# Kernel optimization log

Measured on AMD Instinct MI355X. Metric: run time of the kernel, lower is better.

The kernel has to match this reference:

```python
import jax, jax.numpy as jnp
import numpy as np

B, S, DIM, H = 2, 2048, 1536, 12
HD = DIM // H  # 128
EPS = 1e-6


def setup_inputs() -> dict:
    key = jax.random.key(0)
    ks = jax.random.split(key, 6)
    x = jax.random.normal(ks[0], (B, S, DIM), dtype=jnp.float32)
    # RoPE rotation as (cos, sin) pairs: shape [S, 1, HD//2, 2]
    inv = 1.0 / (10000.0 ** (np.arange(0, HD, 2, dtype=np.float32) / HD))
    ang = np.arange(S, dtype=np.float32)[:, None] * inv[None, :]  # [S, HD//2]
    freqs = jnp.asarray(np.stack([np.cos(ang), np.sin(ang)], axis=-1))[:, None, :, :]
    def lin(k):
        return jax.random.normal(k, (DIM, DIM), dtype=jnp.float32) * 0.02
    wq, wk, wv, wo = lin(ks[1]), lin(ks[2]), lin(ks[3]), lin(ks[4])
    zb = jnp.zeros((DIM,), dtype=jnp.float32)
    ones = jnp.ones((DIM,), dtype=jnp.float32)
    return dict(x=x, freqs=freqs,
                wq=wq, bq=zb, wk=wk, bk=zb, wv=wv, bv=zb, wo=wo, bo=zb,
                gq=ones, gk=ones, timestep=500)


def reference(x, freqs, wq, bq, wk, bk, wv, bv, wo, bo, gq, gk, timestep):
    b, s, dim = x.shape

    def rms(z, g):
        zf = z.astype(jnp.float32)
        n = zf * jax.lax.rsqrt(jnp.mean(zf * zf, axis=-1, keepdims=True) + EPS)
        return n.astype(z.dtype) * g

    def rope(t):
        # [b,s,dim] -> [b,s,H,HD//2,2] pairs; complex multiply by freqs
        tp = t.reshape(b, s, H, HD // 2, 2)
        tr, ti = tp[..., 0], tp[..., 1]
        fr = freqs[None, ..., 0]  # [1,s,1,HD//2] broadcasts over batch & heads
        fi = freqs[None, ..., 1]
        out = jnp.stack([tr * fr - ti * fi, tr * fi + ti * fr], axis=-1)
        return out.reshape(b, s, dim)

    q = rope(rms(x @ wq.T + bq, gq))
    k = rope(rms(x @ wk.T + bk, gk))
    v = x @ wv.T + bv

    qh = q.reshape(b, s, H, HD).transpose(0, 2, 1, 3)
    kh = k.reshape(b, s, H, HD).transpose(0, 2, 1, 3)
    vh = v.reshape(b, s, H, HD).transpose(0, 2, 1, 3)
    scores = jnp.einsum('bhqd,bhkd->bhqk', qh, kh) / np.float32(np.sqrt(HD))
    attn = jax.nn.softmax(scores, axis=-1)
    out = jnp.einsum('bhqk,bhkd->bhqd', attn, vh)
    out = out.transpose(0, 2, 1, 3).reshape(b, s, dim)
    return out @ wo.T + bo
```

## Files before the change

### kernel.cpp

```cpp
#include <hip/hip_runtime.h>
#include <hip/hip_bf16.h>


#define BQ  2
#define SQ  2048
#define DIMQ 1536
#define HQ  12
#define HDQ 128
#define MTOK 4096
#define KDIM 1536

typedef __attribute__((ext_vector_type(8))) short short8;
typedef __attribute__((ext_vector_type(4))) float f32x4;
typedef __attribute__((ext_vector_type(16))) float f32x16;
typedef __attribute__((ext_vector_type(8))) unsigned short u16x8;

typedef __attribute__((address_space(1))) const void global_cvoid;
typedef __attribute__((address_space(3))) void lds_void;

__device__ const float CEc = 0.12751879f;

__device__ __forceinline__ float bf2f(unsigned int u) {
    return __uint_as_float(u << 16);
}
__device__ __forceinline__ unsigned short f2bf(float f) {
    unsigned int u = __float_as_uint(f);
    u += 0x7fffu + ((u >> 16) & 1u);
    return (unsigned short)(u >> 16);
}
__device__ __forceinline__ void gload_lds16(const void* g, void* l) {
    __builtin_amdgcn_global_load_lds((global_cvoid*)g, (lds_void*)l, 16, 0, 0);
}
__device__ __forceinline__ unsigned int cvtpk_bf16(float lo, float hi) {
    unsigned int r;
    asm("v_cvt_pk_bf16_f32 %0, %1, %2" : "=v"(r) : "v"(lo), "v"(hi));
    return r;
}

#define VMCNT(n) asm volatile("s_waitcnt vmcnt(" #n ")" ::: "memory")
#define MEMFENCE() asm volatile("" ::: "memory")
#define BARRIER() do { asm volatile("" ::: "memory"); \
                       __builtin_amdgcn_s_barrier();  \
                       asm volatile("" ::: "memory"); } while (0)

__global__ __launch_bounds__(256)
void cast_all(const float* __restrict__ x,
              const float* __restrict__ wq, const float* __restrict__ wk,
              const float* __restrict__ wv, const float* __restrict__ wo,
              unsigned short* __restrict__ Xb,
              unsigned short* __restrict__ Wqkv,
              unsigned short* __restrict__ Wob)
{
    const int NX = 1572864, NW = 589824;
    int i = blockIdx.x * blockDim.x + threadIdx.x;
    int stride = gridDim.x * blockDim.x;
    for (; i < NX + 4 * NW; i += stride) {
        const float* s; unsigned short* d; int off;
        if (i < NX) { s = x; d = Xb; off = i; }
        else {
            int j = i - NX;
            int seg = j / NW;
            off = j - seg * NW;
            s = (seg == 0) ? wq : (seg == 1) ? wk : (seg == 2) ? wv : wo;
            d = (seg < 3) ? (Wqkv + seg * 2359296) : Wob;
        }
        float4 v = ((const float4*)s)[off];
        unsigned short a = f2bf(v.x), b = f2bf(v.y), c = f2bf(v.z), e = f2bf(v.w);
        unsigned int lo = (unsigned int)a | ((unsigned int)b << 16);
        unsigned int hi = (unsigned int)c | ((unsigned int)e << 16);
        ((uint2*)d)[off] = make_uint2(lo, hi);
    }
}

template<int MODE>
__global__ __launch_bounds__(256)
void gemm_bt(const unsigned short* __restrict__ A,
             const unsigned short* __restrict__ Bm,
             unsigned short* __restrict__ oQ,
             unsigned short* __restrict__ oK,
             unsigned short* __restrict__ oV,
             const float* __restrict__ biasq,
             const float* __restrict__ biask,
             const float* __restrict__ biasv,
             float* __restrict__ oF,
             const float* __restrict__ biaso)
{
    __shared__ unsigned short ldsA[128 * 64];
    __shared__ unsigned short ldsB[128 * 64];
    const int m0 = blockIdx.x * 128;
    const int n0 = blockIdx.y * 128;
    const int t = threadIdx.x;
    const int lane = t & 63;
    const int wid = t >> 6;
    const int wr = (wid >> 1) * 64;
    const int wc = (wid & 1) * 64;
    const int lr = lane & 15;
    const int lk = lane >> 4;

    f32x4 acc[4][4] = {};

    #pragma unroll 1
    for (int kt = 0; kt < KDIM; kt += 64) {
        #pragma unroll
        for (int i = 0; i < 4; ++i) {
            const int off = i * 4096 + wid * 1024 + lane * 16;
            const int r = off >> 7;
            const int c = (off >> 4) & 7;
            const int csw = (c ^ (r & 7)) << 3;
            gload_lds16(A + (size_t)(m0 + r) * KDIM + kt + csw,
                        (char*)ldsA + i * 4096 + wid * 1024);
            gload_lds16(Bm + (size_t)(n0 + r) * KDIM + kt + csw,
                        (char*)ldsB + i * 4096 + wid * 1024);
        }
        __syncthreads();

        #pragma unroll
        for (int kk = 0; kk < 2; ++kk) {
            short8 af[4], bf[4];
            #pragma unroll
            for (int mi = 0; mi < 4; ++mi) {
                int row = wr + mi * 16 + lr;
                int ch = (kk * 4 + lk) ^ (row & 7);
                af[mi] = *(const short8*)((const char*)ldsA + row * 128 + ch * 16);
            }
            #pragma unroll
            for (int ni = 0; ni < 4; ++ni) {
                int row = wc + ni * 16 + lr;
                int ch = (kk * 4 + lk) ^ (row & 7);
                bf[ni] = *(const short8*)((const char*)ldsB + row * 128 + ch * 16);
            }
            #pragma unroll
            for (int mi = 0; mi < 4; ++mi)
                #pragma unroll
                for (int ni = 0; ni < 4; ++ni)
                    acc[mi][ni] = __builtin_amdgcn_mfma_f32_16x16x32_bf16(
                        af[mi], bf[ni], acc[mi][ni], 0, 0, 0);
        }
        __syncthreads();
    }

    if (MODE == 0) {
        const int seg = n0 / 1536;
        unsigned short* op = (seg == 0) ? oQ : (seg == 1 ? oK : oV);
        const float* bp = (seg == 0) ? biasq : (seg == 1 ? biask : biasv);
        const int nl0 = n0 - seg * 1536;
        #pragma unroll
        for (int mi = 0; mi < 4; ++mi)
            #pragma unroll
            for (int ni = 0; ni < 4; ++ni)
                #pragma unroll
                for (int j = 0; j < 4; ++j) {
                    int row = m0 + wr + mi * 16 + lk * 4 + j;
                    int col = nl0 + wc + ni * 16 + lr;
                    op[(size_t)row * 1536 + col] = f2bf(acc[mi][ni][j] + bp[col]);
                }
    } else {
        #pragma unroll
        for (int mi = 0; mi < 4; ++mi)
            #pragma unroll
            for (int ni = 0; ni < 4; ++ni)
                #pragma unroll
                for (int j = 0; j < 4; ++j) {
                    int row = m0 + wr + mi * 16 + lk * 4 + j;
                    int col = n0 + wc + ni * 16 + lr;
                    oF[(size_t)row * 1536 + col] = acc[mi][ni][j] + biaso[col];
                }
    }
}

__global__ __launch_bounds__(256)
void rmsnorm_rope(unsigned short* __restrict__ T,
                  const float* __restrict__ g,
                  const float* __restrict__ freqs)
{
    const int token = blockIdx.x;
    const int s = token & (SQ - 1);
    unsigned int* row = (unsigned int*)(T + (size_t)token * DIMQ);
    const int t = threadIdx.x;
    const int lane = t & 63, wid = t >> 6;

    float pr[3], pi[3];
    float ss = 0.f;
    #pragma unroll
    for (int q = 0; q < 3; ++q) {
        unsigned int v = row[t + q * 256];
        float a = bf2f(v & 0xffffu);
        float b = bf2f(v >> 16);
        pr[q] = a; pi[q] = b;
        ss += a * a + b * b;
    }
    ss += __shfl_xor(ss, 32); ss += __shfl_xor(ss, 16); ss += __shfl_xor(ss, 8);
    ss += __shfl_xor(ss, 4);  ss += __shfl_xor(ss, 2);  ss += __shfl_xor(ss, 1);
    __shared__ float red[4];
    if (lane == 0) red[wid] = ss;
    __syncthreads();
    float tot = red[0] + red[1] + red[2] + red[3];
    float sc = rsqrtf(tot * (1.0f / 1536.0f) + 1e-6f);

    #pragma unroll
    for (int q = 0; q < 3; ++q) {
        int p = t + q * 256;
        int ph = p & 63;
        float fr = freqs[s * 128 + ph * 2];
        float fi = freqs[s * 128 + ph * 2 + 1];
        float nr = pr[q] * sc * g[2 * p];
        float ni = pi[q] * sc * g[2 * p + 1];
        float outr = nr * fr - ni * fi;
        float outi = nr * fi + ni * fr;
        row[p] = (unsigned int)f2bf(outr) | ((unsigned int)f2bf(outi) << 16);
    }
}

__global__ __launch_bounds__(256)
void vtrans(const unsigned short* __restrict__ V, unsigned short* __restrict__ Vt)
{
    __shared__ unsigned short tile[64][72];
    const int s0 = blockIdx.x * 64;
    const int d0 = blockIdx.y * 64;
    const int bh = blockIdx.z;
    const int b = bh / HQ, h = bh % HQ;
    const int t = threadIdx.x;

    #pragma unroll
    for (int i = 0; i < 2; ++i) {
        int cid = i * 256 + t;
        int r = cid >> 3, c = cid & 7;
        u16x8 v = *(const u16x8*)(V + (size_t)(b * SQ + s0 + r) * DIMQ + h * HDQ + d0 + c * 8);
        #pragma unroll
        for (int e = 0; e < 8; ++e) tile[r][c * 8 + e] = v[e];
    }
    __syncthreads();
    #pragma unroll
    for (int i = 0; i < 2; ++i) {
        int cid = i * 256 + t;
        int rd = cid >> 3, c = cid & 7;
        u16x8 w;
        #pragma unroll
        for (int e = 0; e < 8; ++e) w[e] = tile[c * 8 + e][rd];
        *(u16x8*)(Vt + (size_t)(bh * HDQ + d0 + rd) * SQ + s0 + c * 8) = w;
    }
}

__global__ __launch_bounds__(128)
void attn(const unsigned short* __restrict__ Q,
          const unsigned short* __restrict__ Kb,
          const unsigned short* __restrict__ Vt,
          unsigned short* __restrict__ Op0,
          unsigned short* __restrict__ Op1,
          float* __restrict__ ml)
{
    __shared__ char smem[24576];
    char* Kl0 = smem;
    char* Kl1 = smem + 8192;
    char* Vl  = smem + 16384;

    const int fid = blockIdx.x;
    const int xcd = fid & 7;
    const int slot = fid >> 3;
    const int bh = xcd * 3 + (slot >> 6);
    const int r64 = slot & 63;
    const int qt = r64 >> 1;
    const int sp = r64 & 1;
    const int b = bh / HQ, h = bh % HQ;

    const int t = threadIdx.x;
    const int lane = t & 63, wid = t >> 6;
    const int l31 = lane & 31, hi = lane >> 5;
    const int s0q = qt * 64 + wid * 32;
    const int f = (bh * 32 + qt) * 2 + wid;
    const int kvbeg = sp * 1024, kvend = kvbeg + 1024;
    const float THR = 90.5f;

    const unsigned short* Kbase = Kb + (size_t)(b * SQ) * DIMQ + h * HDQ;
    const unsigned short* Vbase = Vt + (size_t)(bh * HDQ) * SQ;

    short8 qf[8];
    {
        const unsigned short* qp = Q + (size_t)(b * SQ + s0q + l31) * DIMQ + h * HDQ;
        #pragma unroll
        for (int kc = 0; kc < 8; ++kc)
            qf[kc] = *(const short8*)(qp + kc * 16 + hi * 8);
    }
    MEMFENCE();
    #pragma unroll
    for (int i = 0; i < 4; ++i) {
        const int j = wid * 4 + i;
        const int off = j * 1024 + lane * 16;
        int r = off >> 8, c = (off >> 4) & 15;
        gload_lds16(Kbase + (size_t)(kvbeg + r) * DIMQ + ((c ^ (r & 7)) << 3),
                    Kl0 + j * 1024);
    }
    VMCNT(4);

    char* kcur = Kl0;
    char* knxt = Kl1;
    float mrun = -1e30f, lsum = 0.f, nm = 1e30f;
    f32x16 oacc[4] = {};

    #pragma unroll 1
    for (int kv0 = kvbeg; kv0 < kvend; kv0 += 32) {
        #pragma unroll
        for (int i = 0; i < 4; ++i) {
            const int j = wid * 4 + i;
            const int off = j * 1024 + lane * 16;
            int r = off >> 6, c = (off >> 4) & 3;
            gload_lds16(Vbase + (size_t)r * SQ + kv0 + ((c ^ ((r >> 1) & 3)) << 3),
                        Vl + j * 1024);
        }
        MEMFENCE();
        const int kvn = (kv0 + 32 < SQ) ? kv0 + 32 : kv0;
        #pragma unroll
        for (int i = 0; i < 4; ++i) {
            const int j = wid * 4 + i;
            const int off = j * 1024 + lane * 16;
            int r = off >> 8, c = (off >> 4) & 15;
            gload_lds16(Kbase + (size_t)(kvn + r) * DIMQ + ((c ^ (r & 7)) << 3),
                        knxt + j * 1024);
        }

        VMCNT(8);
        BARRIER();

        f32x16 sa = {}, sb = {};
        const int rb = l31 * 256;
        const int rx = l31 & 7;
        __builtin_amdgcn_s_setprio(1);
        #pragma unroll
        for (int kc = 0; kc < 4; ++kc) {
            short8 kf = *(const short8*)(kcur + rb + (((kc * 2 + hi) ^ rx) << 4));
            sa = __builtin_amdgcn_mfma_f32_32x32x16_bf16(kf, qf[kc], sa, 0, 0, 0);
        }
        #pragma unroll
        for (int kc = 4; kc < 8; ++kc) {
            short8 kf = *(const short8*)(kcur + rb + (((kc * 2 + hi) ^ rx) << 4));
            sb = __builtin_amdgcn_mfma_f32_32x32x16_bf16(kf, qf[kc], sb, 0, 0, 0);
        }
        __builtin_amdgcn_s_setprio(0);
        f32x16 s;
        #pragma unroll
        for (int r = 0; r < 16; ++r) s[r] = sa[r] + sb[r];

        float mt[8];
        #pragma unroll
        for (int r = 0; r < 8; ++r) mt[r] = fmaxf(s[r], s[r + 8]);
        #pragma unroll
        for (int st = 4; st > 0; st >>= 1)
            #pragma unroll
            for (int r = 0; r < 4; ++r)
                if (r < st) mt[r] = fmaxf(mt[r], mt[r + st]);
        float tm = fmaxf(mt[0], __shfl_xor(mt[0], 32));
        if (!__all(tm <= mrun + THR)) {
            float mnew = fmaxf(mrun, tm);
            float al = __builtin_amdgcn_exp2f((mrun - mnew) * CEc);
            lsum *= al;
            #pragma unroll
            for (int dt = 0; dt < 4; ++dt)
                #pragma unroll
                for (int r = 0; r < 16; ++r) oacc[dt][r] *= al;
            mrun = mnew;
            nm = -mrun * CEc;
        }
        float rs = 0.f;
        #pragma unroll
        for (int r = 0; r < 16; ++r) {
            float p = __builtin_amdgcn_exp2f(__builtin_fmaf(s[r], CEc, nm));
            s[r] = p; rs += p;
        }
        lsum += rs;

        unsigned int A0 = cvtpk_bf16(s[0], s[1]),  A1 = cvtpk_bf16(s[2], s[3]);
        unsigned int B0 = cvtpk_bf16(s[4], s[5]),  B1 = cvtpk_bf16(s[6], s[7]);
        unsigned int C0 = cvtpk_bf16(s[8], s[9]),  C1 = cvtpk_bf16(s[10], s[11]);
        unsigned int D0 = cvtpk_bf16(s[12], s[13]), D1 = cvtpk_bf16(s[14], s[15]);
        unsigned int xA0 = __shfl_xor(A0, 32), xA1 = __shfl_xor(A1, 32);
        unsigned int xB0 = __shfl_xor(B0, 32), xB1 = __shfl_xor(B1, 32);
        unsigned int xC0 = __shfl_xor(C0, 32), xC1 = __shfl_xor(C1, 32);
        unsigned int xD0 = __shfl_xor(D0, 32), xD1 = __shfl_xor(D1, 32);
        union { unsigned int w[4]; short8 v; } pf0, pf1;
        pf0.w[0] = hi ? xB0 : A0;  pf0.w[1] = hi ? xB1 : A1;
        pf0.w[2] = hi ? B0 : xA0;  pf0.w[3] = hi ? B1 : xA1;
        pf1.w[0] = hi ? xD0 : C0;  pf1.w[1] = hi ? xD1 : C1;
        pf1.w[2] = hi ? D0 : xC0;  pf1.w[3] = hi ? D1 : xC1;

        VMCNT(4);
        BARRIER();

        __builtin_amdgcn_s_setprio(1);
        #pragma unroll
        for (int dt = 0; dt < 4; ++dt) {
            const int drow = dt * 32 + l31;
            const int sw = (drow >> 1) & 3;
            short8 v0 = *(const short8*)(Vl + drow * 64 + ((hi ^ sw) << 4));
            short8 v1 = *(const short8*)(Vl + drow * 64 + (((2 + hi) ^ sw) << 4));
            oacc[dt] = __builtin_amdgcn_mfma_f32_32x32x16_bf16(v0, pf0.v, oacc[dt], 0, 0, 0);
            oacc[dt] = __builtin_amdgcn_mfma_f32_32x32x16_bf16(v1, pf1.v, oacc[dt], 0, 0, 0);
        }
        __builtin_amdgcn_s_setprio(0);

        BARRIER();

        char* tp = kcur; kcur = knxt; knxt = tp;
    }

    float ltot = lsum + __shfl_xor(lsum, 32);
    float rnl = 1.0f / ltot;
    unsigned short* Op = sp ? Op1 : Op0;
    #pragma unroll
    for (int dt = 0; dt < 4; ++dt) {
        unsigned int w[8];
        #pragma unroll
        for (int j = 0; j < 8; ++j)
            w[j] = (unsigned int)f2bf(oacc[dt][2 * j] * rnl)
                 | ((unsigned int)f2bf(oacc[dt][2 * j + 1] * rnl) << 16);
        *(uint4*)(Op + (size_t)f * 4096 + (dt * 2 + 0) * 512 + lane * 8) =
            make_uint4(w[0], w[1], w[2], w[3]);
        *(uint4*)(Op + (size_t)f * 4096 + (dt * 2 + 1) * 512 + lane * 8) =
            make_uint4(w[4], w[5], w[6], w[7]);
    }
    ml[(size_t)(sp * 1536 + f) * 128 + lane] = mrun;
    ml[(size_t)(sp * 1536 + f) * 128 + 64 + lane] = ltot;
}

__global__ __launch_bounds__(256)
void attn_combine(const unsigned short* __restrict__ Op0,
                  const unsigned short* __restrict__ Op1,
                  const float* __restrict__ ml,
                  unsigned short* __restrict__ Ao)
{
    __shared__ char smem[32768];
    const int f = blockIdx.x * 4 + (threadIdx.x >> 6);
    const int lane = threadIdx.x & 63;
    const int l31 = lane & 31, hi = lane >> 5;
    const int bh = f >> 6, qt = (f >> 1) & 31, wid = f & 1;
    const int b = bh / HQ, h = bh % HQ;
    const int s0q = qt * 64 + wid * 32;

    float m0 = ml[(size_t)f * 128 + lane];
    float l0 = ml[(size_t)f * 128 + 64 + lane];
    float m1 = ml[(size_t)(1536 + f) * 128 + lane];
    float l1 = ml[(size_t)(1536 + f) * 128 + 64 + lane];
    float ms = fmaxf(m0, m1);
    float w0 = __builtin_amdgcn_exp2f((m0 - ms) * CEc) * l0;
    float w1 = __builtin_amdgcn_exp2f((m1 - ms) * CEc) * l1;
    float rL = 1.0f / (w0 + w1);
    float a0 = w0 * rL, a1 = w1 * rL;

    char* Ot = smem + (threadIdx.x >> 6) * 8192;
    #pragma unroll
    for (int dt = 0; dt < 4; ++dt)
        #pragma unroll
        for (int hf = 0; hf < 2; ++hf) {
            u16x8 o0 = *(const u16x8*)(Op0 + (size_t)f * 4096 + (dt * 2 + hf) * 512 + lane * 8);
            u16x8 o1 = *(const u16x8*)(Op1 + (size_t)f * 4096 + (dt * 2 + hf) * 512 + lane * 8);
            #pragma unroll
            for (int j = 0; j < 4; ++j) {
                int r = hf * 8 + 2 * j;
                float v0 = a0 * bf2f((unsigned short)o0[2 * j])     + a1 * bf2f((unsigned short)o1[2 * j]);
                float v1 = a0 * bf2f((unsigned short)o0[2 * j + 1]) + a1 * bf2f((unsigned short)o1[2 * j + 1]);
                int d = dt * 32 + (r & 3) + 8 * (r >> 2) + 4 * hi;
                unsigned int w = (unsigned int)f2bf(v0) | ((unsigned int)f2bf(v1) << 16);
                *(unsigned int*)(Ot + l31 * 256 + (((d >> 3) ^ (l31 & 7)) << 4) + (d & 7) * 2) = w;
            }
        }
    #pragma unroll
    for (int ii = 0; ii < 8; ++ii) {
        int task = ii * 64 + lane;
        int q = task >> 4, c = task & 15;
        u16x8 vv = *(const u16x8*)(Ot + q * 256 + ((c ^ (q & 7)) << 4));
        int tok = b * SQ + s0q + q;
        *(u16x8*)(Ao + (size_t)tok * DIMQ + h * HDQ + c * 8) = vv;
    }
}

extern "C" void kernel_launch(void* const* d_in, const int* in_sizes, int n_in,
                              void* d_out, int out_size, void* d_ws, size_t ws_size,
                              hipStream_t stream) {
    (void)in_sizes; (void)n_in; (void)out_size; (void)ws_size;
    const float* x     = (const float*)d_in[0];
    const float* freqs = (const float*)d_in[1];
    const float* wq = (const float*)d_in[2];
    const float* bq = (const float*)d_in[3];
    const float* wk = (const float*)d_in[4];
    const float* bk = (const float*)d_in[5];
    const float* wv = (const float*)d_in[6];
    const float* bv = (const float*)d_in[7];
    const float* wo = (const float*)d_in[8];
    const float* bo = (const float*)d_in[9];
    const float* gq = (const float*)d_in[10];
    const float* gk = (const float*)d_in[11];
    float* out = (float*)d_out;

    char* w = (char*)d_ws;
    unsigned short* Xb   = (unsigned short*)(w);
    unsigned short* Wqkv = (unsigned short*)(w + 12582912);
    unsigned short* Wob  = (unsigned short*)(w + 26738688);
    unsigned short* Qb   = (unsigned short*)(w + 31457280);
    unsigned short* Kbuf = (unsigned short*)(w + 44040192);
    unsigned short* Vb   = (unsigned short*)(w + 56623104);
    unsigned short* Vt   = (unsigned short*)(w + 69206016);
    unsigned short* Ao   = Xb;
    unsigned short* Op0  = Wqkv;
    float*          mlbf = (float*)(w + 25165824);
    unsigned short* Op1  = Vb;

    cast_all<<<2048, 256, 0, stream>>>(x, wq, wk, wv, wo, Xb, Wqkv, Wob);

    gemm_bt<0><<<dim3(32, 36), 256, 0, stream>>>(
        Xb, Wqkv, Qb, Kbuf, Vb, bq, bk, bv, nullptr, nullptr);

    rmsnorm_rope<<<4096, 256, 0, stream>>>(Qb,   gq, freqs);
    rmsnorm_rope<<<4096, 256, 0, stream>>>(Kbuf, gk, freqs);
    vtrans<<<dim3(32, 2, 24), 256, 0, stream>>>(Vb, Vt);

    attn<<<1536, 128, 0, stream>>>(Qb, Kbuf, Vt, Op0, Op1, mlbf);
    attn_combine<<<384, 256, 0, stream>>>(Op0, Op1, mlbf, Ao);

    gemm_bt<1><<<dim3(32, 12), 256, 0, stream>>>(
        Ao, Wob, nullptr, nullptr, nullptr, nullptr, nullptr, nullptr, out, bo);
}
```

Baseline: 259.2 us.

## Use single-wave attention blocks with register V loads and merge rmsnorm launches

Restructures the attention kernel so each block is one 64-lane wave handling 32 query rows, with twice as many blocks. V fragments are loaded straight from global memory into registers instead of staged through LDS, which removes all block barriers and the priority hints. The two rmsnorm_rope launches are merged into one 2D grid. The trade-off is that K tiles are no longer shared between two waves, so global K traffic per query doubles, and the direct V loads are strided with no LDS staging.

Result: slower. 331.4 us (+27.9%).

```diff
diff --git a/kernel.cpp b/kernel.cpp
--- a/kernel.cpp
+++ b/kernel.cpp
@@ -39,9 +39,6 @@
 
 #define VMCNT(n) asm volatile("s_waitcnt vmcnt(" #n ")" ::: "memory")
 #define MEMFENCE() asm volatile("" ::: "memory")
-#define BARRIER() do { asm volatile("" ::: "memory"); \
-                       __builtin_amdgcn_s_barrier();  \
-                       asm volatile("" ::: "memory"); } while (0)
 
 __global__ __launch_bounds__(256)
 void cast_all(const float* __restrict__ x,
@@ -169,10 +166,14 @@
 }
 
 __global__ __launch_bounds__(256)
-void rmsnorm_rope(unsigned short* __restrict__ T,
-                  const float* __restrict__ g,
+void rmsnorm_rope(unsigned short* __restrict__ Qb,
+                  unsigned short* __restrict__ Kb,
+                  const float* __restrict__ gq,
+                  const float* __restrict__ gk,
                   const float* __restrict__ freqs)
 {
+    unsigned short* T = blockIdx.y ? Kb : Qb;
+    const float* g = blockIdx.y ? gk : gq;
     const int token = blockIdx.x;
     const int s = token & (SQ - 1);
     unsigned int* row = (unsigned int*)(T + (size_t)token * DIMQ);
@@ -241,7 +242,7 @@
     }
 }
 
-__global__ __launch_bounds__(128)
+__global__ __launch_bounds__(64)
 void attn(const unsigned short* __restrict__ Q,
           const unsigned short* __restrict__ Kb,
           const unsigned short* __restrict__ Vt,
@@ -249,27 +250,25 @@
           unsigned short* __restrict__ Op1,
           float* __restrict__ ml)
 {
-    __shared__ char smem[24576];
+    __shared__ char smem[16384];
     char* Kl0 = smem;
     char* Kl1 = smem + 8192;
-    char* Vl  = smem + 16384;
 
     const int fid = blockIdx.x;
     const int xcd = fid & 7;
     const int slot = fid >> 3;
-    const int bh = xcd * 3 + (slot >> 6);
-    const int r64 = slot & 63;
-    const int qt = r64 >> 1;
-    const int sp = r64 & 1;
+    const int bh = xcd * 3 + (slot >> 7);
+    const int rem = slot & 127;
+    const int qtile = rem >> 1;
+    const int sp = rem & 1;
     const int b = bh / HQ, h = bh % HQ;
-
-    const int t = threadIdx.x;
-    const int lane = t & 63, wid = t >> 6;
-    const int l31 = lane & 31, hi = lane >> 5;
-    const int s0q = qt * 64 + wid * 32;
-    const int f = (bh * 32 + qt) * 2 + wid;
+    const int s0q = qtile * 32;
+    const int f = bh * 64 + qtile;
     const int kvbeg = sp * 1024, kvend = kvbeg + 1024;
     const float THR = 90.5f;
+
+    const int lane = threadIdx.x;
+    const int l31 = lane & 31, hi = lane >> 5;
 
     const unsigned short* Kbase = Kb + (size_t)(b * SQ) * DIMQ + h * HDQ;
     const unsigned short* Vbase = Vt + (size_t)(bh * HDQ) * SQ;
@@ -283,14 +282,13 @@
     }
     MEMFENCE();
     #pragma unroll
-    for (int i = 0; i < 4; ++i) {
-        const int j = wid * 4 + i;
-        const int off = j * 1024 + lane * 16;
+    for (int i = 0; i < 8; ++i) {
+        const int off = i * 1024 + lane * 16;
         int r = off >> 8, c = (off >> 4) & 15;
         gload_lds16(Kbase + (size_t)(kvbeg + r) * DIMQ + ((c ^ (r & 7)) << 3),
-                    Kl0 + j * 1024);
-    }
-    VMCNT(4);
+                    Kl0 + i * 1024);
+    }
+    MEMFENCE();
 
     char* kcur = Kl0;
     char* knxt = Kl1;
@@ -299,32 +297,28 @@
 
     #pragma unroll 1
     for (int kv0 = kvbeg; kv0 < kvend; kv0 += 32) {
-        #pragma unroll
-        for (int i = 0; i < 4; ++i) {
-            const int j = wid * 4 + i;
-            const int off = j * 1024 + lane * 16;
-            int r = off >> 6, c = (off >> 4) & 3;
-            gload_lds16(Vbase + (size_t)r * SQ + kv0 + ((c ^ ((r >> 1) & 3)) << 3),
-                        Vl + j * 1024);
-        }
+        short8 vr[4][2];
+        #pragma unroll
+        for (int dt = 0; dt < 4; ++dt)
+            #pragma unroll
+            for (int j = 0; j < 2; ++j)
+                vr[dt][j] = *(const short8*)(Vbase + (size_t)(dt * 32 + l31) * SQ
+                                             + kv0 + j * 16 + hi * 8);
         MEMFENCE();
         const int kvn = (kv0 + 32 < SQ) ? kv0 + 32 : kv0;
         #pragma unroll
-        for (int i = 0; i < 4; ++i) {
-            const int j = wid * 4 + i;
-            const int off = j * 1024 + lane * 16;
+        for (int i = 0; i < 8; ++i) {
+            const int off = i * 1024 + lane * 16;
             int r = off >> 8, c = (off >> 4) & 15;
             gload_lds16(Kbase + (size_t)(kvn + r) * DIMQ + ((c ^ (r & 7)) << 3),
-                        knxt + j * 1024);
-        }
-
-        VMCNT(8);
-        BARRIER();
+                        knxt + i * 1024);
+        }
+
+        VMCNT(16);
 
         f32x16 sa = {}, sb = {};
         const int rb = l31 * 256;
         const int rx = l31 & 7;
-        __builtin_amdgcn_s_setprio(1);
         #pragma unroll
         for (int kc = 0; kc < 4; ++kc) {
             short8 kf = *(const short8*)(kcur + rb + (((kc * 2 + hi) ^ rx) << 4));
@@ -335,7 +329,6 @@
             short8 kf = *(const short8*)(kcur + rb + (((kc * 2 + hi) ^ rx) << 4));
             sb = __builtin_amdgcn_mfma_f32_32x32x16_bf16(kf, qf[kc], sb, 0, 0, 0);
         }
-        __builtin_amdgcn_s_setprio(0);
         f32x16 s;
         #pragma unroll
         for (int r = 0; r < 16; ++r) s[r] = sa[r] + sb[r];
@@ -382,22 +375,13 @@
         pf1.w[0] = hi ? xD0 : C0;  pf1.w[1] = hi ? xD1 : C1;
         pf1.w[2] = hi ? D0 : xC0;  pf1.w[3] = hi ? D1 : xC1;
 
-        VMCNT(4);
-        BARRIER();
-
-        __builtin_amdgcn_s_setprio(1);
+        VMCNT(8);
+
         #pragma unroll
         for (int dt = 0; dt < 4; ++dt) {
-            const int drow = dt * 32 + l31;
-            const int sw = (drow >> 1) & 3;
-            short8 v0 = *(const short8*)(Vl + drow * 64 + ((hi ^ sw) << 4));
-            short8 v1 = *(const short8*)(Vl + drow * 64 + (((2 + hi) ^ sw) << 4));
-            oacc[dt] = __builtin_amdgcn_mfma_f32_32x32x16_bf16(v0, pf0.v, oacc[dt], 0, 0, 0);
-            oacc[dt] = __builtin_amdgcn_mfma_f32_32x32x16_bf16(v1, pf1.v, oacc[dt], 0, 0, 0);
-        }
-        __builtin_amdgcn_s_setprio(0);
-
-        BARRIER();
+            oacc[dt] = __builtin_amdgcn_mfma_f32_32x32x16_bf16(vr[dt][0], pf0.v, oacc[dt], 0, 0, 0);
+            oacc[dt] = __builtin_amdgcn_mfma_f32_32x32x16_bf16(vr[dt][1], pf1.v, oacc[dt], 0, 0, 0);
+        }
 
         char* tp = kcur; kcur = knxt; knxt = tp;
     }
@@ -431,9 +415,9 @@
     const int f = blockIdx.x * 4 + (threadIdx.x >> 6);
     const int lane = threadIdx.x & 63;
     const int l31 = lane & 31, hi = lane >> 5;
-    const int bh = f >> 6, qt = (f >> 1) & 31, wid = f & 1;
+    const int bh = f >> 6;
     const int b = bh / HQ, h = bh % HQ;
-    const int s0q = qt * 64 + wid * 32;
+    const int s0q = (f & 63) * 32;
 
     float m0 = ml[(size_t)f * 128 + lane];
     float l0 = ml[(size_t)f * 128 + 64 + lane];
@@ -508,11 +492,10 @@
     gemm_bt<0><<<dim3(32, 36), 256, 0, stream>>>(
         Xb, Wqkv, Qb, Kbuf, Vb, bq, bk, bv, nullptr, nullptr);
 
-    rmsnorm_rope<<<4096, 256, 0, stream>>>(Qb,   gq, freqs);
-    rmsnorm_rope<<<4096, 256, 0, stream>>>(Kbuf, gk, freqs);
+    rmsnorm_rope<<<dim3(4096, 2), 256, 0, stream>>>(Qb, Kbuf, gq, gk, freqs);
     vtrans<<<dim3(32, 2, 24), 256, 0, stream>>>(Vb, Vt);
 
-    attn<<<1536, 128, 0, stream>>>(Qb, Kbuf, Vt, Op0, Op1, mlbf);
+    attn<<<3072, 64, 0, stream>>>(Qb, Kbuf, Vt, Op0, Op1, mlbf);
     attn_combine<<<384, 256, 0, stream>>>(Op0, Op1, mlbf, Ao);
 
     gemm_bt<1><<<dim3(32, 12), 256, 0, stream>>>(
```
